# Kernel tuning notes

Hardware: AMD Instinct MI355X
Metric: run time of the kernel (lower is better)

## Reference

```python
import jax, jax.numpy as jnp
import numpy as np

N_HEADS = 32
N_KV_HEADS = 8
HEAD_DIM = 64
ROPE_THETA = 10000.0
NEG_INF = -1e9


def apply_rope(t, offset=0):
    # t: [B, H, L, hd]; half-split (rotate-half) RoPE convention
    B, H, L, hd = t.shape
    pos = jnp.arange(offset, offset + L, dtype=jnp.float32)            # [L]
    inv_freq = 1.0 / (ROPE_THETA ** (jnp.arange(0, hd, 2, dtype=jnp.float32) / hd))  # [hd/2]
    ang = pos[:, None] * inv_freq[None, :]                              # [L, hd/2]
    cos = jnp.cos(ang).astype(t.dtype)
    sin = jnp.sin(ang).astype(t.dtype)
    t1, t2 = jnp.split(t, 2, axis=-1)                                   # each [B,H,L,hd/2]
    return jnp.concatenate([t1 * cos - t2 * sin, t1 * sin + t2 * cos], axis=-1)


def setup_inputs() -> dict:
    key = jax.random.key(0)
    ks = jax.random.split(key, 6)
    B, L, D = 1, 2048, 2048
    x = jax.random.normal(ks[0], (B, L, D), dtype=jnp.float32)
    attn_scale = jnp.ones((1,), dtype=jnp.float32)
    # causal additive mask: 0 on/below diagonal, -1e9 above
    mask = jnp.where(jnp.tril(jnp.ones((L, L), dtype=bool)), 0.0, NEG_INF).astype(jnp.float32)
    s = 0.02
    Wq = jax.random.normal(ks[1], (N_HEADS * HEAD_DIM, D), dtype=jnp.float32) * s
    Wk = jax.random.normal(ks[2], (N_KV_HEADS * HEAD_DIM, D), dtype=jnp.float32) * s
    Wv = jax.random.normal(ks[3], (N_KV_HEADS * HEAD_DIM, D), dtype=jnp.float32) * s
    Wo = jax.random.normal(ks[4], (D, N_HEADS * HEAD_DIM), dtype=jnp.float32) * s
    return {"x": x, "attn_scale": attn_scale, "mask": mask,
            "Wq": Wq, "Wk": Wk, "Wv": Wv, "Wo": Wo}


def reference(x, attn_scale, mask, Wq, Wk, Wv, Wo):
    B, L, D = x.shape
    scale = HEAD_DIM ** -0.5
    # projections (nn.Linear: y = x @ W.T)
    q = (x @ Wq.T).reshape(B, L, N_HEADS, HEAD_DIM).transpose(0, 2, 1, 3)     # [B,H,L,hd]
    k = (x @ Wk.T).reshape(B, L, N_KV_HEADS, HEAD_DIM).transpose(0, 2, 1, 3)  # [B,Hk,L,hd]
    v = (x @ Wv.T).reshape(B, L, N_KV_HEADS, HEAD_DIM).transpose(0, 2, 1, 3)
    q = apply_rope(q)
    k = apply_rope(k)
    q = q * attn_scale  # elementwise attn_scale applied to queries
    # GQA: repeat kv heads
    rep = N_HEADS // N_KV_HEADS
    k = jnp.repeat(k, rep, axis=1)
    v = jnp.repeat(v, rep, axis=1)
    scores = jnp.einsum('bhld,bhmd->bhlm', q, k) * scale + mask
    probs = jax.nn.softmax(scores, axis=-1)
    out = jnp.einsum('bhlm,bhmd->bhld', probs, v)          # [B,H,L,hd]
    out = out.transpose(0, 2, 1, 3).reshape(B, L, N_HEADS * HEAD_DIM)
    return out @ Wo.T
```

## Files before the change

kernel.cpp:

```cpp
#include <hip/hip_runtime.h>
#include <stdint.h>

typedef short bf16x8 __attribute__((ext_vector_type(8)));
typedef float f32x4 __attribute__((ext_vector_type(4)));

__device__ __forceinline__ unsigned short f2bf(float f) {
  uint32_t u = __float_as_uint(f);
  u = (u + 0x7FFFu + ((u >> 16) & 1u)) >> 16;
  return (unsigned short)u;
}
__device__ __forceinline__ float bf2f(unsigned short h) {
  return __uint_as_float(((uint32_t)h) << 16);
}

__device__ __forceinline__ void gload16(const void* g, void* lds) {
  const __attribute__((address_space(1))) char* gp =
      (const __attribute__((address_space(1))) char*)(uintptr_t)g;
  __attribute__((address_space(3))) char* sp =
      (__attribute__((address_space(3))) char*)(uint32_t)(uintptr_t)lds;
  __builtin_amdgcn_global_load_lds(gp, sp, 16, 0, 0);
}

__global__ void k_cvt_all(const float* __restrict__ x, const float* __restrict__ Wq,
                          const float* __restrict__ Wk, const float* __restrict__ Wv,
                          const float* __restrict__ Wo, unsigned short* __restrict__ xb,
                          unsigned short* __restrict__ Wcat, unsigned short* __restrict__ Wob) {
  int b = blockIdx.x;
  const float* src;
  unsigned short* dst;
  int off;
  if (b < 4096)       { src = x;  dst = xb;                  off = b; }
  else if (b < 8192)  { src = Wq; dst = Wcat;                off = b - 4096; }
  else if (b < 9216)  { src = Wk; dst = Wcat + 2048 * 2048;  off = b - 8192; }
  else if (b < 10240) { src = Wv; dst = Wcat + 2560 * 2048;  off = b - 9216; }
  else                { src = Wo; dst = Wob;                  off = b - 10240; }
  int i = off * 256 + threadIdx.x;
  float4 v = ((const float4*)src)[i];
  ushort4 o;
  o.x = f2bf(v.x); o.y = f2bf(v.y); o.z = f2bf(v.z); o.w = f2bf(v.w);
  ((ushort4*)dst)[i] = o;
}

template <int OUTF32, int ROPE>
__global__ __launch_bounds__(256) void k_gemm(const unsigned short* __restrict__ A,
                                              const unsigned short* __restrict__ B,
                                              void* __restrict__ Cout,
                                              int M, int N, int K,
                                              const float* __restrict__ scale_p) {
  __shared__ unsigned short As[2][128 * 64];
  __shared__ unsigned short Bs[2][128 * 64];
  const int tid = threadIdx.x;
  const int w = tid >> 6, lane = tid & 63;
  const int g = lane >> 4, cl = lane & 15;
  const int nTn = N >> 7;
  const int per = gridDim.x >> 3;
  const int bid = (blockIdx.x & 7) * per + (blockIdx.x >> 3);
  const int tm = bid / nTn, tn = bid % nTn;
  const int m0 = tm << 7, n0 = tn << 7;
  const int wm = (w >> 1) << 6, wn = (w & 1) << 6;
  f32x4 acc[4][4] = {};

  auto stage = [&](int kt, int b) {
#pragma unroll
    for (int it = 0; it < 8; ++it) {
      int cc = tid + it * 256;
      int half = cc >> 10;
      int c3 = cc & 1023;
      int row = c3 >> 3, kb = (c3 & 7) << 4;
      const unsigned short* base = half ? (B + (size_t)(n0 + row) * K + kt)
                                        : (A + (size_t)(m0 + row) * K + kt);
      const char* src = (const char*)base + (kb ^ ((row & 7) << 4));
      char* dstl = (char*)(half ? Bs[b] : As[b]) + c3 * 16;
      gload16(src, dstl);
    }
  };

  stage(0, 0);
  asm volatile("s_waitcnt vmcnt(0)" ::: "memory");
  __syncthreads();
  int buf = 0;

  for (int kt = 0; kt < K; kt += 64) {
    if (kt + 64 < K) stage(kt + 64, buf ^ 1);
#pragma unroll
    for (int ks = 0; ks < 2; ++ks) {
      bf16x8 af[4], bfr[4];
#pragma unroll
      for (int i = 0; i < 4; ++i) {
        int row = wm + i * 16 + cl;
        int kb = ((g << 4) + (ks << 6)) ^ ((row & 7) << 4);
        af[i] = *(const bf16x8*)((const char*)As[buf] + row * 128 + kb);
      }
#pragma unroll
      for (int j = 0; j < 4; ++j) {
        int row = wn + j * 16 + cl;
        int kb = ((g << 4) + (ks << 6)) ^ ((row & 7) << 4);
        bfr[j] = *(const bf16x8*)((const char*)Bs[buf] + row * 128 + kb);
      }
#pragma unroll
      for (int i = 0; i < 4; ++i)
#pragma unroll
        for (int j = 0; j < 4; ++j)
          acc[i][j] = __builtin_amdgcn_mfma_f32_16x16x32_bf16(af[i], bfr[j], acc[i][j], 0, 0, 0);
    }
    asm volatile("s_waitcnt vmcnt(0)" ::: "memory");
    __syncthreads();
    buf ^= 1;
  }

  if (ROPE && n0 < 2560) {
    float s0v = scale_p[0] * 0.125f * 1.4426950408889634f;
    float sc = (n0 < 2048) ? s0v : 1.0f;
    float invf[2];
#pragma unroll
    for (int j = 0; j < 2; ++j)
      invf[j] = __expf(-(float)(j * 16 + cl) * 0.2878231366242557f);
#pragma unroll
    for (int i = 0; i < 4; ++i)
#pragma unroll
      for (int r = 0; r < 4; ++r) {
        float pos = (float)(m0 + wm + i * 16 + (g << 2) + r);
#pragma unroll
        for (int j = 0; j < 2; ++j) {
          float ang = pos * invf[j];
          float sn, cs;
          __sincosf(ang, &sn, &cs);
          float t1 = acc[i][j][r], t2 = acc[i][j + 2][r];
          acc[i][j][r] = (t1 * cs - t2 * sn) * sc;
          acc[i][j + 2][r] = (t1 * sn + t2 * cs) * sc;
        }
      }
  }

#pragma unroll
  for (int i = 0; i < 4; ++i)
#pragma unroll
    for (int j = 0; j < 4; ++j)
#pragma unroll
      for (int r = 0; r < 4; ++r) {
        int row = m0 + wm + i * 16 + (g << 2) + r;
        int col = n0 + wn + j * 16 + cl;
        float v = acc[i][j][r];
        if (OUTF32)
          ((float*)Cout)[(size_t)row * N + col] = v;
        else
          ((unsigned short*)Cout)[(size_t)row * N + col] = f2bf(v);
      }
}

__global__ void k_vt(const unsigned short* __restrict__ qkv, unsigned short* __restrict__ vt) {
  __shared__ unsigned short tl[64][80];
  const int tid = threadIdx.x;
  const int hk = blockIdx.x >> 5, lt = blockIdx.x & 31;
  const int l0 = lt << 6;
#pragma unroll
  for (int it = 0; it < 2; ++it) {
    int cc = tid + it * 256;
    int lr = cc >> 3, d0 = (cc & 7) << 3;
    uint4 v = *(const uint4*)(qkv + (size_t)(l0 + lr) * 3072 + 2560 + hk * 64 + d0);
    *(uint4*)&tl[lr][d0] = v;
  }
  __syncthreads();
#pragma unroll
  for (int it = 0; it < 2; ++it) {
    int cc = tid + it * 256;
    int dr = cc >> 3, le = (cc & 7) << 3;
    unsigned short tmp[8] __attribute__((aligned(16)));
#pragma unroll
    for (int j = 0; j < 8; ++j) tmp[j] = tl[le + j][dr];
    *(uint4*)(vt + (size_t)(hk * 64 + dr) * 2048 + l0 + le) = *(const uint4*)tmp;
  }
}

__global__ __launch_bounds__(256) void k_attn(const unsigned short* __restrict__ qkv,
                                              const unsigned short* __restrict__ vt,
                                              unsigned short* __restrict__ ao) {
  __shared__ unsigned short Ks[2][64 * 64];
  __shared__ unsigned short Vs[2][64 * 64];
  __shared__ unsigned short Ps[4 * 16 * 64];
  const int tid = threadIdx.x;
  const int w = tid >> 6, lane = tid & 63;
  const int g = lane >> 4, cl = lane & 15;
  const int h = blockIdx.x & 31;
  const int qb = 31 - (blockIdx.x >> 5);
  const int q0 = qb << 6;
  const int hk = h >> 2;
  const int qg = q0 + w * 16 + cl;

  const unsigned short* qptr = qkv + (size_t)qg * 3072 + h * 64 + g * 8;
  bf16x8 qf0 = *(const bf16x8*)qptr;
  bf16x8 qf1 = *(const bf16x8*)(qptr + 32);

  float m_run = -3e38f, l_run = 0.0f;
  f32x4 acc[4] = {};

  const unsigned short* kbase = qkv + 2048 + hk * 64;
  const unsigned short* vbase = vt + (size_t)hk * 64 * 2048;
  char* myP = (char*)Ps + w * 2048;

  auto stageK = [&](int ck, int b) {
    const int kv0 = ck << 6;
#pragma unroll
    for (int it = 0; it < 2; ++it) {
      int cc = tid + it * 256;
      int row = cc >> 3, kb = (cc & 7) << 4;
      const char* src = (const char*)(kbase + (size_t)(kv0 + row) * 3072) + (kb ^ ((row & 7) << 4));
      gload16(src, (char*)Ks[b] + cc * 16);
    }
  };
  auto stageV = [&](int ck, int b) {
    const int kv0 = ck << 6;
#pragma unroll
    for (int it = 0; it < 2; ++it) {
      int cc = tid + it * 256;
      int row = cc >> 3, kb = (cc & 7) << 4;
      const char* src = (const char*)(vbase + (size_t)row * 2048 + kv0) + (kb ^ ((row & 7) << 4));
      gload16(src, (char*)Vs[b] + cc * 16);
    }
  };

  stageK(0, 0); stageV(0, 0);
  if (qb >= 1) stageK(1, 1);
  asm volatile("s_waitcnt vmcnt(0)" ::: "memory");
  __syncthreads();

  float svP[4][4];
  {
    const char* Kc = (const char*)Ks[0];
    __builtin_amdgcn_s_setprio(1);
#pragma unroll
    for (int t = 0; t < 4; ++t) {
      f32x4 st = {};
#pragma unroll
      for (int ks = 0; ks < 2; ++ks) {
        int row = t * 16 + cl;
        int kb = ((g << 4) + (ks << 6)) ^ ((row & 7) << 4);
        bf16x8 kf = *(const bf16x8*)(Kc + row * 128 + kb);
        st = __builtin_amdgcn_mfma_f32_16x16x32_bf16(kf, ks ? qf1 : qf0, st, 0, 0, 0);
      }
#pragma unroll
      for (int r = 0; r < 4; ++r) svP[t][r] = st[r];
    }
    __builtin_amdgcn_s_setprio(0);
  }
  __syncthreads();

  for (int i = 0; i <= qb; ++i) {
    if (i + 2 <= qb) stageK(i + 2, i & 1);
    if (i + 1 <= qb) stageV(i + 1, (i + 1) & 1);

    float svN[4][4];
    if (i < qb) {
      const char* Kc = (const char*)Ks[(i + 1) & 1];
      __builtin_amdgcn_s_setprio(1);
#pragma unroll
      for (int t = 0; t < 4; ++t) {
        f32x4 st = {};
#pragma unroll
        for (int ks = 0; ks < 2; ++ks) {
          int row = t * 16 + cl;
          int kb = ((g << 4) + (ks << 6)) ^ ((row & 7) << 4);
          bf16x8 kf = *(const bf16x8*)(Kc + row * 128 + kb);
          st = __builtin_amdgcn_mfma_f32_16x16x32_bf16(kf, ks ? qf1 : qf0, st, 0, 0, 0);
        }
#pragma unroll
        for (int r = 0; r < 4; ++r) svN[t][r] = st[r];
      }
      __builtin_amdgcn_s_setprio(0);
    }

    if (i == qb) {
      const int kv0 = i << 6;
#pragma unroll
      for (int t = 0; t < 4; ++t)
#pragma unroll
        for (int r = 0; r < 4; ++r) {
          int kvg = kv0 + t * 16 + (g << 2) + r;
          if (kvg > qg) svP[t][r] = -1e9f;
        }
    }
    float pm[4];
#pragma unroll
    for (int t = 0; t < 4; ++t)
      pm[t] = fmaxf(fmaxf(svP[t][0], svP[t][1]), fmaxf(svP[t][2], svP[t][3]));
    float pmax = fmaxf(fmaxf(pm[0], pm[1]), fmaxf(pm[2], pm[3]));
    pmax = fmaxf(pmax, __shfl_xor(pmax, 16));
    pmax = fmaxf(pmax, __shfl_xor(pmax, 32));
    if (!__all(pmax - m_run <= 8.0f)) {
      float m_new = fmaxf(m_run, pmax);
      float fac = __builtin_exp2f(m_run - m_new);
      float fr[4];
#pragma unroll
      for (int r = 0; r < 4; ++r) fr[r] = __shfl(fac, (g << 2) + r);
#pragma unroll
      for (int t = 0; t < 4; ++t) {
        acc[t][0] *= fr[0]; acc[t][1] *= fr[1]; acc[t][2] *= fr[2]; acc[t][3] *= fr[3];
      }
      l_run *= fac;
      m_run = m_new;
    }
    float ps[4];
#pragma unroll
    for (int t = 0; t < 4; ++t) {
      float e0 = __builtin_exp2f(svP[t][0] - m_run);
      float e1 = __builtin_exp2f(svP[t][1] - m_run);
      float e2 = __builtin_exp2f(svP[t][2] - m_run);
      float e3 = __builtin_exp2f(svP[t][3] - m_run);
      ps[t] = (e0 + e1) + (e2 + e3);
      uint32_t d0, d1;
      asm("v_cvt_pk_bf16_f32 %0, %1, %2" : "=v"(d0) : "v"(e0), "v"(e1));
      asm("v_cvt_pk_bf16_f32 %0, %1, %2" : "=v"(d1) : "v"(e2), "v"(e3));
      uint2 dd; dd.x = d0; dd.y = d1;
      int kb = ((t << 5) + (g << 3)) ^ ((cl & 7) << 4);
      *(uint2*)(myP + cl * 128 + kb) = dd;
    }
    float psum = (ps[0] + ps[1]) + (ps[2] + ps[3]);
    psum += __shfl_xor(psum, 16);
    psum += __shfl_xor(psum, 32);
    l_run += psum;

    {
      const char* Vc = (const char*)Vs[i & 1];
      __builtin_amdgcn_s_setprio(1);
#pragma unroll
      for (int ks = 0; ks < 2; ++ks) {
        int kbp = ((g << 4) + (ks << 6)) ^ ((cl & 7) << 4);
        bf16x8 pf = *(const bf16x8*)(myP + cl * 128 + kbp);
#pragma unroll
        for (int t = 0; t < 4; ++t) {
          int row = t * 16 + cl;
          int kbv = ((g << 4) + (ks << 6)) ^ ((row & 7) << 4);
          bf16x8 vf = *(const bf16x8*)(Vc + row * 128 + kbv);
          acc[t] = __builtin_amdgcn_mfma_f32_16x16x32_bf16(pf, vf, acc[t], 0, 0, 0);
        }
      }
      __builtin_amdgcn_s_setprio(0);
    }

    if (i < qb) {
      asm volatile("s_waitcnt vmcnt(0)" ::: "memory");
      __syncthreads();
#pragma unroll
      for (int t = 0; t < 4; ++t)
#pragma unroll
        for (int r = 0; r < 4; ++r) svP[t][r] = svN[t][r];
    }
  }

  float li[4];
#pragma unroll
  for (int r = 0; r < 4; ++r) li[r] = 1.0f / __shfl(l_run, (g << 2) + r);
#pragma unroll
  for (int t = 0; t < 4; ++t)
#pragma unroll
    for (int r = 0; r < 4; ++r) {
      int row = q0 + w * 16 + (g << 2) + r;
      int col = h * 64 + t * 16 + cl;
      ao[(size_t)row * 2048 + col] = f2bf(acc[t][r] * li[r]);
    }
}

extern "C" void kernel_launch(void* const* d_in, const int* in_sizes, int n_in,
                              void* d_out, int out_size, void* d_ws, size_t ws_size,
                              hipStream_t stream) {
  (void)in_sizes; (void)n_in; (void)out_size; (void)ws_size;
  const float* x  = (const float*)d_in[0];
  const float* sc = (const float*)d_in[1];
  const float* Wq = (const float*)d_in[3];
  const float* Wk = (const float*)d_in[4];
  const float* Wv = (const float*)d_in[5];
  const float* Wo = (const float*)d_in[6];
  float* out = (float*)d_out;
  char* ws = (char*)d_ws;
  unsigned short* xb   = (unsigned short*)(ws);
  unsigned short* Wcat = (unsigned short*)(ws + 8388608);
  unsigned short* Wob  = (unsigned short*)(ws + 20971520);
  unsigned short* QKV  = (unsigned short*)(ws + 29360128);
  unsigned short* VT   = (unsigned short*)(ws + 41943040);
  unsigned short* AO   = (unsigned short*)(ws + 44040192);

  k_cvt_all<<<14336, 256, 0, stream>>>(x, Wq, Wk, Wv, Wo, xb, Wcat, Wob);
  k_gemm<0, 1><<<384, 256, 0, stream>>>(xb, Wcat, QKV, 2048, 3072, 2048, sc);
  k_vt<<<256, 256, 0, stream>>>(QKV, VT);
  k_attn<<<1024, 256, 0, stream>>>(QKV, VT, AO);
  k_gemm<1, 0><<<256, 256, 0, stream>>>(AO, Wob, out, 2048, 2048, 2048, nullptr);
}
```

Measured before the change: 126.0 us.

## Split KV range of long causal query blocks and merge partials in combine kernel

The 512 attention blocks with the most causal key tiles (query blocks 16-31) are each split into two halves over the KV range. Each half writes unnormalised fp32 accumulators plus the running max and sum to workspace, and a new combine kernel merges the pairs with a log-sum-exp rescale. The goal is to even out per-block work and fill the GPU better in the causal attention kernel. The cost is an extra kernel launch and extra partial-result traffic, and the partial buffers reuse workspace that held the bf16 inputs and weights of the earlier projection GEMM.

```diff
diff --git a/kernel.cpp b/kernel.cpp
--- a/kernel.cpp
+++ b/kernel.cpp
@@ -174,15 +174,35 @@
 
 __global__ __launch_bounds__(256) void k_attn(const unsigned short* __restrict__ qkv,
                                               const unsigned short* __restrict__ vt,
-                                              unsigned short* __restrict__ ao) {
+                                              unsigned short* __restrict__ ao,
+                                              float* __restrict__ partAcc,
+                                              float* __restrict__ partML) {
   __shared__ unsigned short Ks[2][64 * 64];
   __shared__ unsigned short Vs[2][64 * 64];
   __shared__ unsigned short Ps[4 * 16 * 64];
   const int tid = threadIdx.x;
   const int w = tid >> 6, lane = tid & 63;
   const int g = lane >> 4, cl = lane & 15;
-  const int h = blockIdx.x & 31;
-  const int qb = 31 - (blockIdx.x >> 5);
+  const int b = blockIdx.x;
+  const int h = b & 31;
+  const int u = b >> 5;
+  int qb, lo, hi, part;
+  bool split;
+  if (u < 32) {
+    qb = 16 + (u >> 1);
+    part = u & 1;
+    int mid = (qb + 2) >> 1;
+    lo = part ? mid : 0;
+    hi = part ? (qb + 1) : mid;
+    split = true;
+  } else {
+    qb = 47 - u;
+    lo = 0;
+    hi = qb + 1;
+    split = false;
+    part = 0;
+  }
+  const int nt = hi - lo;
   const int q0 = qb << 6;
   const int hk = h >> 2;
   const int qg = q0 + w * 16 + cl;
@@ -198,29 +218,29 @@
   const unsigned short* vbase = vt + (size_t)hk * 64 * 2048;
   char* myP = (char*)Ps + w * 2048;
 
-  auto stageK = [&](int ck, int b) {
+  auto stageK = [&](int ck, int bb) {
     const int kv0 = ck << 6;
 #pragma unroll
     for (int it = 0; it < 2; ++it) {
       int cc = tid + it * 256;
       int row = cc >> 3, kb = (cc & 7) << 4;
       const char* src = (const char*)(kbase + (size_t)(kv0 + row) * 3072) + (kb ^ ((row & 7) << 4));
-      gload16(src, (char*)Ks[b] + cc * 16);
+      gload16(src, (char*)Ks[bb] + cc * 16);
     }
   };
-  auto stageV = [&](int ck, int b) {
+  auto stageV = [&](int ck, int bb) {
     const int kv0 = ck << 6;
 #pragma unroll
     for (int it = 0; it < 2; ++it) {
       int cc = tid + it * 256;
       int row = cc >> 3, kb = (cc & 7) << 4;
       const char* src = (const char*)(vbase + (size_t)row * 2048 + kv0) + (kb ^ ((row & 7) << 4));
-      gload16(src, (char*)Vs[b] + cc * 16);
+      gload16(src, (char*)Vs[bb] + cc * 16);
     }
   };
 
-  stageK(0, 0); stageV(0, 0);
-  if (qb >= 1) stageK(1, 1);
+  stageK(lo, 0); stageV(lo, 0);
+  if (nt >= 2) stageK(lo + 1, 1);
   asm volatile("s_waitcnt vmcnt(0)" ::: "memory");
   __syncthreads();
 
@@ -245,12 +265,13 @@
   }
   __syncthreads();
 
-  for (int i = 0; i <= qb; ++i) {
-    if (i + 2 <= qb) stageK(i + 2, i & 1);
-    if (i + 1 <= qb) stageV(i + 1, (i + 1) & 1);
+  for (int i = 0; i < nt; ++i) {
+    const int tile = lo + i;
+    if (i + 2 < nt) stageK(lo + i + 2, i & 1);
+    if (i + 1 < nt) stageV(lo + i + 1, (i + 1) & 1);
 
     float svN[4][4];
-    if (i < qb) {
+    if (i + 1 < nt) {
       const char* Kc = (const char*)Ks[(i + 1) & 1];
       __builtin_amdgcn_s_setprio(1);
 #pragma unroll
@@ -269,8 +290,8 @@
       __builtin_amdgcn_s_setprio(0);
     }
 
-    if (i == qb) {
-      const int kv0 = i << 6;
+    if (tile == qb) {
+      const int kv0 = tile << 6;
 #pragma unroll
       for (int t = 0; t < 4; ++t)
 #pragma unroll
@@ -337,7 +358,7 @@
       __builtin_amdgcn_s_setprio(0);
     }
 
-    if (i < qb) {
+    if (i + 1 < nt) {
       asm volatile("s_waitcnt vmcnt(0)" ::: "memory");
       __syncthreads();
 #pragma unroll
@@ -347,17 +368,64 @@
     }
   }
 
-  float li[4];
-#pragma unroll
-  for (int r = 0; r < 4; ++r) li[r] = 1.0f / __shfl(l_run, (g << 2) + r);
-#pragma unroll
-  for (int t = 0; t < 4; ++t)
-#pragma unroll
-    for (int r = 0; r < 4; ++r) {
-      int row = q0 + w * 16 + (g << 2) + r;
-      int col = h * 64 + t * 16 + cl;
-      ao[(size_t)row * 2048 + col] = f2bf(acc[t][r] * li[r]);
-    }
+  if (!split) {
+    float li[4];
+#pragma unroll
+    for (int r = 0; r < 4; ++r) li[r] = 1.0f / __shfl(l_run, (g << 2) + r);
+#pragma unroll
+    for (int t = 0; t < 4; ++t)
+#pragma unroll
+      for (int r = 0; r < 4; ++r) {
+        int row = q0 + w * 16 + (g << 2) + r;
+        int col = h * 64 + t * 16 + cl;
+        ao[(size_t)row * 2048 + col] = f2bf(acc[t][r] * li[r]);
+      }
+  } else {
+    const int idx = (((h << 4) + (qb - 16)) << 1) + part;
+    float* pa = partAcc + (size_t)idx * 4096;
+    float* pml = partML + idx * 128;
+#pragma unroll
+    for (int t = 0; t < 4; ++t)
+#pragma unroll
+      for (int r = 0; r < 4; ++r)
+        pa[(w * 16 + (g << 2) + r) * 64 + t * 16 + cl] = acc[t][r];
+    if (g == 0) {
+      pml[w * 16 + cl] = m_run;
+      pml[64 + w * 16 + cl] = l_run;
+    }
+  }
+}
+
+__global__ __launch_bounds__(256) void k_combine(const float* __restrict__ partAcc,
+                                                 const float* __restrict__ partML,
+                                                 unsigned short* __restrict__ ao) {
+  const int b = blockIdx.x;
+  const int h = b & 31, qi = b >> 5;
+  const int qb = 16 + qi;
+  const int base = (((h << 4) + qi) << 1);
+  const float* a0 = partAcc + (size_t)base * 4096;
+  const float* a1 = a0 + 4096;
+  const float* ml0 = partML + base * 128;
+  const float* ml1 = ml0 + 128;
+  const int t = threadIdx.x;
+  const int q = t >> 2, d0 = (t & 3) << 4;
+  float m0 = ml0[q], m1 = ml1[q], l0 = ml0[64 + q], l1 = ml1[64 + q];
+  float m = fmaxf(m0, m1);
+  float f0 = __builtin_exp2f(m0 - m), f1 = __builtin_exp2f(m1 - m);
+  float li = 1.0f / (l0 * f0 + l1 * f1);
+  unsigned short tmp[16] __attribute__((aligned(16)));
+#pragma unroll
+  for (int j = 0; j < 16; j += 4) {
+    float4 v0 = *(const float4*)(a0 + q * 64 + d0 + j);
+    float4 v1 = *(const float4*)(a1 + q * 64 + d0 + j);
+    tmp[j + 0] = f2bf((v0.x * f0 + v1.x * f1) * li);
+    tmp[j + 1] = f2bf((v0.y * f0 + v1.y * f1) * li);
+    tmp[j + 2] = f2bf((v0.z * f0 + v1.z * f1) * li);
+    tmp[j + 3] = f2bf((v0.w * f0 + v1.w * f1) * li);
+  }
+  size_t orow = (size_t)(qb * 64 + q) * 2048 + h * 64 + d0;
+  *(uint4*)(ao + orow) = *(const uint4*)tmp;
+  *(uint4*)(ao + orow + 8) = *(const uint4*)(tmp + 8);
 }
 
 extern "C" void kernel_launch(void* const* d_in, const int* in_sizes, int n_in,
@@ -378,10 +446,13 @@
   unsigned short* QKV  = (unsigned short*)(ws + 29360128);
   unsigned short* VT   = (unsigned short*)(ws + 41943040);
   unsigned short* AO   = (unsigned short*)(ws + 44040192);
+  float* partAcc = (float*)(ws);
+  float* partML  = (float*)(ws + 16777216);
 
   k_cvt_all<<<14336, 256, 0, stream>>>(x, Wq, Wk, Wv, Wo, xb, Wcat, Wob);
   k_gemm<0, 1><<<384, 256, 0, stream>>>(xb, Wcat, QKV, 2048, 3072, 2048, sc);
   k_vt<<<256, 256, 0, stream>>>(QKV, VT);
-  k_attn<<<1024, 256, 0, stream>>>(QKV, VT, AO);
+  k_attn<<<1536, 256, 0, stream>>>(QKV, VT, AO, partAcc, partML);
+  k_combine<<<512, 256, 0, stream>>>(partAcc, partML, AO);
   k_gemm<1, 0><<<256, 256, 0, stream>>>(AO, Wob, out, 2048, 2048, 2048, nullptr);
 }
```

After: 131.3 us. +4.2%, slower.

## Fuse fp32-to-bf16 conversion into GEMM tile loads, dropping the conversion kernel

Applied to the files above, without the earlier changes.

Removes the standalone conversion kernel that wrote bf16 copies of x and all weights. Both GEMMs now load fp32 tiles into registers, convert them with packed bf16 conversion instructions, and write the swizzled result to LDS. This avoids a full extra pass over the inputs and one kernel launch. The cost is that each tile is re-read as fp32 many times across blocks, doubling global and L2 traffic per tile compared with bf16, and staging now goes through registers rather than direct global-to-LDS loads, which adds register pressure and reduces latency hiding.

```diff
diff --git a/kernel.cpp b/kernel.cpp
--- a/kernel.cpp
+++ b/kernel.cpp
@@ -8,9 +8,6 @@
   uint32_t u = __float_as_uint(f);
   u = (u + 0x7FFFu + ((u >> 16) & 1u)) >> 16;
   return (unsigned short)u;
-}
-__device__ __forceinline__ float bf2f(unsigned short h) {
-  return __uint_as_float(((uint32_t)h) << 16);
 }
 
 __device__ __forceinline__ void gload16(const void* g, void* lds) {
@@ -21,32 +18,24 @@
   __builtin_amdgcn_global_load_lds(gp, sp, 16, 0, 0);
 }
 
-__global__ void k_cvt_all(const float* __restrict__ x, const float* __restrict__ Wq,
-                          const float* __restrict__ Wk, const float* __restrict__ Wv,
-                          const float* __restrict__ Wo, unsigned short* __restrict__ xb,
-                          unsigned short* __restrict__ Wcat, unsigned short* __restrict__ Wob) {
-  int b = blockIdx.x;
-  const float* src;
-  unsigned short* dst;
-  int off;
-  if (b < 4096)       { src = x;  dst = xb;                  off = b; }
-  else if (b < 8192)  { src = Wq; dst = Wcat;                off = b - 4096; }
-  else if (b < 9216)  { src = Wk; dst = Wcat + 2048 * 2048;  off = b - 8192; }
-  else if (b < 10240) { src = Wv; dst = Wcat + 2560 * 2048;  off = b - 9216; }
-  else                { src = Wo; dst = Wob;                  off = b - 10240; }
-  int i = off * 256 + threadIdx.x;
-  float4 v = ((const float4*)src)[i];
-  ushort4 o;
-  o.x = f2bf(v.x); o.y = f2bf(v.y); o.z = f2bf(v.z); o.w = f2bf(v.w);
-  ((ushort4*)dst)[i] = o;
-}
-
-template <int OUTF32, int ROPE>
-__global__ __launch_bounds__(256) void k_gemm(const unsigned short* __restrict__ A,
-                                              const unsigned short* __restrict__ B,
-                                              void* __restrict__ Cout,
-                                              int M, int N, int K,
-                                              const float* __restrict__ scale_p) {
+__device__ __forceinline__ void cvt_write16(void* lds_dst, const float4& v0, const float4& v1) {
+  uint32_t w0, w1, w2, w3;
+  asm("v_cvt_pk_bf16_f32 %0, %1, %2" : "=v"(w0) : "v"(v0.x), "v"(v0.y));
+  asm("v_cvt_pk_bf16_f32 %0, %1, %2" : "=v"(w1) : "v"(v0.z), "v"(v0.w));
+  asm("v_cvt_pk_bf16_f32 %0, %1, %2" : "=v"(w2) : "v"(v1.x), "v"(v1.y));
+  asm("v_cvt_pk_bf16_f32 %0, %1, %2" : "=v"(w3) : "v"(v1.z), "v"(v1.w));
+  union { uint32_t u[4]; bf16x8 v; } pw;
+  pw.u[0] = w0; pw.u[1] = w1; pw.u[2] = w2; pw.u[3] = w3;
+  *(bf16x8*)lds_dst = pw.v;
+}
+
+__global__ __launch_bounds__(256) void k_gemm0(const float* __restrict__ Af,
+                                               const float* __restrict__ Bq,
+                                               const float* __restrict__ Bk,
+                                               const float* __restrict__ Bv,
+                                               unsigned short* __restrict__ Cout,
+                                               const float* __restrict__ scale_p) {
+  const int K = 2048, N = 3072;
   __shared__ unsigned short As[2][128 * 64];
   __shared__ unsigned short Bs[2][128 * 64];
   const int tid = threadIdx.x;
@@ -60,28 +49,46 @@
   const int wm = (w >> 1) << 6, wn = (w & 1) << 6;
   f32x4 acc[4][4] = {};
 
-  auto stage = [&](int kt, int b) {
+  float4 st[8][2];
+  auto issue = [&](int kt) {
+#pragma unroll
+    for (int it = 0; it < 8; ++it) {
+      int cc = tid + it * 256;
+      int half = cc >> 10;
+      int c3 = cc & 1023;
+      int row = c3 >> 3, ke = (c3 & 7) << 3;
+      const float* s;
+      if (!half) {
+        s = Af + (size_t)(m0 + row) * K + kt + ke;
+      } else {
+        int n = n0 + row;
+        s = (n < 2048 ? Bq + (size_t)n * K
+                      : n < 2560 ? Bk + (size_t)(n - 2048) * K
+                                 : Bv + (size_t)(n - 2560) * K) + kt + ke;
+      }
+      st[it][0] = *(const float4*)s;
+      st[it][1] = *(const float4*)(s + 4);
+    }
+  };
+  auto writeL = [&](int b) {
 #pragma unroll
     for (int it = 0; it < 8; ++it) {
       int cc = tid + it * 256;
       int half = cc >> 10;
       int c3 = cc & 1023;
       int row = c3 >> 3, kb = (c3 & 7) << 4;
-      const unsigned short* base = half ? (B + (size_t)(n0 + row) * K + kt)
-                                        : (A + (size_t)(m0 + row) * K + kt);
-      const char* src = (const char*)base + (kb ^ ((row & 7) << 4));
-      char* dstl = (char*)(half ? Bs[b] : As[b]) + c3 * 16;
-      gload16(src, dstl);
-    }
-  };
-
-  stage(0, 0);
-  asm volatile("s_waitcnt vmcnt(0)" ::: "memory");
+      char* dst = (char*)(half ? Bs[b] : As[b]) + row * 128 + (kb ^ ((row & 7) << 4));
+      cvt_write16(dst, st[it][0], st[it][1]);
+    }
+  };
+
+  issue(0);
+  writeL(0);
   __syncthreads();
   int buf = 0;
 
   for (int kt = 0; kt < K; kt += 64) {
-    if (kt + 64 < K) stage(kt + 64, buf ^ 1);
+    if (kt + 64 < K) issue(kt + 64);
 #pragma unroll
     for (int ks = 0; ks < 2; ++ks) {
       bf16x8 af[4], bfr[4];
@@ -103,12 +110,12 @@
         for (int j = 0; j < 4; ++j)
           acc[i][j] = __builtin_amdgcn_mfma_f32_16x16x32_bf16(af[i], bfr[j], acc[i][j], 0, 0, 0);
     }
-    asm volatile("s_waitcnt vmcnt(0)" ::: "memory");
+    if (kt + 64 < K) writeL(buf ^ 1);
     __syncthreads();
     buf ^= 1;
   }
 
-  if (ROPE && n0 < 2560) {
+  if (n0 < 2560) {
     float s0v = scale_p[0] * 0.125f * 1.4426950408889634f;
     float sc = (n0 < 2048) ? s0v : 1.0f;
     float invf[2];
@@ -140,11 +147,98 @@
       for (int r = 0; r < 4; ++r) {
         int row = m0 + wm + i * 16 + (g << 2) + r;
         int col = n0 + wn + j * 16 + cl;
-        float v = acc[i][j][r];
-        if (OUTF32)
-          ((float*)Cout)[(size_t)row * N + col] = v;
-        else
-          ((unsigned short*)Cout)[(size_t)row * N + col] = f2bf(v);
+        Cout[(size_t)row * N + col] = f2bf(acc[i][j][r]);
+      }
+}
+
+__global__ __launch_bounds__(256) void k_gemm1(const unsigned short* __restrict__ A,
+                                               const float* __restrict__ Bf,
+                                               float* __restrict__ Cout) {
+  const int K = 2048, N = 2048;
+  __shared__ unsigned short As[2][128 * 64];
+  __shared__ unsigned short Bs[2][128 * 64];
+  const int tid = threadIdx.x;
+  const int w = tid >> 6, lane = tid & 63;
+  const int g = lane >> 4, cl = lane & 15;
+  const int nTn = N >> 7;
+  const int per = gridDim.x >> 3;
+  const int bid = (blockIdx.x & 7) * per + (blockIdx.x >> 3);
+  const int tm = bid / nTn, tn = bid % nTn;
+  const int m0 = tm << 7, n0 = tn << 7;
+  const int wm = (w >> 1) << 6, wn = (w & 1) << 6;
+  f32x4 acc[4][4] = {};
+
+  float4 st[4][2];
+  auto issue = [&](int kt, int b) {
+#pragma unroll
+    for (int it = 0; it < 4; ++it) {
+      int c3 = tid + it * 256;
+      int row = c3 >> 3, kb = (c3 & 7) << 4;
+      const char* src = (const char*)(A + (size_t)(m0 + row) * K + kt) + (kb ^ ((row & 7) << 4));
+      gload16(src, (char*)As[b] + c3 * 16);
+    }
+#pragma unroll
+    for (int it = 0; it < 4; ++it) {
+      int c3 = tid + it * 256;
+      int row = c3 >> 3, ke = (c3 & 7) << 3;
+      const float* s = Bf + (size_t)(n0 + row) * K + kt + ke;
+      st[it][0] = *(const float4*)s;
+      st[it][1] = *(const float4*)(s + 4);
+    }
+  };
+  auto writeL = [&](int b) {
+#pragma unroll
+    for (int it = 0; it < 4; ++it) {
+      int c3 = tid + it * 256;
+      int row = c3 >> 3, kb = (c3 & 7) << 4;
+      char* dst = (char*)Bs[b] + row * 128 + (kb ^ ((row & 7) << 4));
+      cvt_write16(dst, st[it][0], st[it][1]);
+    }
+  };
+
+  issue(0, 0);
+  writeL(0);
+  asm volatile("s_waitcnt vmcnt(0)" ::: "memory");
+  __syncthreads();
+  int buf = 0;
+
+  for (int kt = 0; kt < K; kt += 64) {
+    if (kt + 64 < K) issue(kt + 64, buf ^ 1);
+#pragma unroll
+    for (int ks = 0; ks < 2; ++ks) {
+      bf16x8 af[4], bfr[4];
+#pragma unroll
+      for (int i = 0; i < 4; ++i) {
+        int row = wm + i * 16 + cl;
+        int kb = ((g << 4) + (ks << 6)) ^ ((row & 7) << 4);
+        af[i] = *(const bf16x8*)((const char*)As[buf] + row * 128 + kb);
+      }
+#pragma unroll
+      for (int j = 0; j < 4; ++j) {
+        int row = wn + j * 16 + cl;
+        int kb = ((g << 4) + (ks << 6)) ^ ((row & 7) << 4);
+        bfr[j] = *(const bf16x8*)((const char*)Bs[buf] + row * 128 + kb);
+      }
+#pragma unroll
+      for (int i = 0; i < 4; ++i)
+#pragma unroll
+        for (int j = 0; j < 4; ++j)
+          acc[i][j] = __builtin_amdgcn_mfma_f32_16x16x32_bf16(af[i], bfr[j], acc[i][j], 0, 0, 0);
+    }
+    if (kt + 64 < K) writeL(buf ^ 1);
+    asm volatile("s_waitcnt vmcnt(0)" ::: "memory");
+    __syncthreads();
+    buf ^= 1;
+  }
+#pragma unroll
+  for (int i = 0; i < 4; ++i)
+#pragma unroll
+    for (int j = 0; j < 4; ++j)
+#pragma unroll
+      for (int r = 0; r < 4; ++r) {
+        int row = m0 + wm + i * 16 + (g << 2) + r;
+        int col = n0 + wn + j * 16 + cl;
+        Cout[(size_t)row * N + col] = acc[i][j][r];
       }
 }
 
@@ -230,16 +324,16 @@
     __builtin_amdgcn_s_setprio(1);
 #pragma unroll
     for (int t = 0; t < 4; ++t) {
-      f32x4 st = {};
+      f32x4 stv = {};
 #pragma unroll
       for (int ks = 0; ks < 2; ++ks) {
         int row = t * 16 + cl;
         int kb = ((g << 4) + (ks << 6)) ^ ((row & 7) << 4);
         bf16x8 kf = *(const bf16x8*)(Kc + row * 128 + kb);
-        st = __builtin_amdgcn_mfma_f32_16x16x32_bf16(kf, ks ? qf1 : qf0, st, 0, 0, 0);
-      }
-#pragma unroll
-      for (int r = 0; r < 4; ++r) svP[t][r] = st[r];
+        stv = __builtin_amdgcn_mfma_f32_16x16x32_bf16(kf, ks ? qf1 : qf0, stv, 0, 0, 0);
+      }
+#pragma unroll
+      for (int r = 0; r < 4; ++r) svP[t][r] = stv[r];
     }
     __builtin_amdgcn_s_setprio(0);
   }
@@ -255,16 +349,16 @@
       __builtin_amdgcn_s_setprio(1);
 #pragma unroll
       for (int t = 0; t < 4; ++t) {
-        f32x4 st = {};
+        f32x4 stv = {};
 #pragma unroll
         for (int ks = 0; ks < 2; ++ks) {
           int row = t * 16 + cl;
           int kb = ((g << 4) + (ks << 6)) ^ ((row & 7) << 4);
           bf16x8 kf = *(const bf16x8*)(Kc + row * 128 + kb);
-          st = __builtin_amdgcn_mfma_f32_16x16x32_bf16(kf, ks ? qf1 : qf0, st, 0, 0, 0);
+          stv = __builtin_amdgcn_mfma_f32_16x16x32_bf16(kf, ks ? qf1 : qf0, stv, 0, 0, 0);
         }
 #pragma unroll
-        for (int r = 0; r < 4; ++r) svN[t][r] = st[r];
+        for (int r = 0; r < 4; ++r) svN[t][r] = stv[r];
       }
       __builtin_amdgcn_s_setprio(0);
     }
@@ -372,16 +466,12 @@
   const float* Wo = (const float*)d_in[6];
   float* out = (float*)d_out;
   char* ws = (char*)d_ws;
-  unsigned short* xb   = (unsigned short*)(ws);
-  unsigned short* Wcat = (unsigned short*)(ws + 8388608);
-  unsigned short* Wob  = (unsigned short*)(ws + 20971520);
-  unsigned short* QKV  = (unsigned short*)(ws + 29360128);
-  unsigned short* VT   = (unsigned short*)(ws + 41943040);
-  unsigned short* AO   = (unsigned short*)(ws + 44040192);
-
-  k_cvt_all<<<14336, 256, 0, stream>>>(x, Wq, Wk, Wv, Wo, xb, Wcat, Wob);
-  k_gemm<0, 1><<<384, 256, 0, stream>>>(xb, Wcat, QKV, 2048, 3072, 2048, sc);
+  unsigned short* QKV = (unsigned short*)(ws);
+  unsigned short* VT  = (unsigned short*)(ws + 12582912);
+  unsigned short* AO  = (unsigned short*)(ws + 14680064);
+
+  k_gemm0<<<384, 256, 0, stream>>>(x, Wq, Wk, Wv, QKV, sc);
   k_vt<<<256, 256, 0, stream>>>(QKV, VT);
   k_attn<<<1024, 256, 0, stream>>>(QKV, VT, AO);
-  k_gemm<1, 0><<<256, 256, 0, stream>>>(AO, Wob, out, 2048, 2048, 2048, nullptr);
-}
+  k_gemm1<<<256, 256, 0, stream>>>(AO, Wo, out);
+}
```

Result: slower. 150.3 us (+19.3%).
